# Performance work log

Measured on AMD Instinct MI355X. Metric: run time of the kernel, lower is better.

## Reference

```python
import jax, jax.numpy as jnp
import numpy as np

# loss weights (match init_kwargs)
L_M, L_U, L_B, L_D = 1.0, 7.0, 2.0, 1.0
NV, NP, NI, NB = 500_000, 64, 48, 2  # voxels, predictions, instances, batches


def setup_inputs() -> dict:
    key = jax.random.key(0)
    k1, k2 = jax.random.split(key)
    logits = jax.random.normal(k1, (NV, NP), dtype=jnp.float32)
    # sorted batch ids per voxel (first half batch 0, second half batch 1)
    voxel_batch = (jnp.arange(NV) * NB // NV).astype(jnp.int32)
    per_b = NI // NB
    # instance ids consistent with voxel batch (module assumes one batch per instance)
    gt_ids = (voxel_batch * per_b + jax.random.randint(k2, (NV,), 0, per_b)).astype(jnp.int32)
    centroid_batches = (jnp.arange(NP) * NB // NP).astype(jnp.int32)
    return {"logits": logits, "voxel_batch": voxel_batch, "gt_ids": gt_ids,
            "centroid_batches": centroid_batches}


def linear_sum_assignment(cost):
    """Hungarian algorithm (e-maxx JV variant) on a small numpy cost matrix."""
    cost = np.asarray(cost, dtype=np.float64)
    transposed = cost.shape[0] > cost.shape[1]
    C = cost.T if transposed else cost
    n, m = C.shape
    u = np.zeros(n + 1); v = np.zeros(m + 1)
    p = np.zeros(m + 1, dtype=np.int64); way = np.zeros(m + 1, dtype=np.int64)
    for i in range(1, n + 1):
        p[0] = i; j0 = 0
        minv = np.full(m + 1, np.inf); used = np.zeros(m + 1, dtype=bool)
        while True:
            used[j0] = True
            i0 = p[j0]; j1 = 0; delta = np.inf
            for j in range(1, m + 1):
                if not used[j]:
                    cur = C[i0 - 1, j - 1] - u[i0] - v[j]
                    if cur < minv[j]:
                        minv[j] = cur; way[j] = j0
                    if minv[j] < delta:
                        delta = minv[j]; j1 = j
            for j in range(m + 1):
                if used[j]:
                    u[p[j]] += delta; v[j] -= delta
                else:
                    minv[j] -= delta
            j0 = j1
            if p[j0] == 0:
                break
        while j0:
            j1 = way[j0]; p[j0] = p[j1]; j0 = j1
    ans = np.zeros(n, dtype=np.int64)
    for j in range(1, m + 1):
        if p[j] > 0:
            ans[p[j] - 1] = j - 1
    rows, cols = np.arange(n), ans
    if transposed:
        rows, cols = cols, rows
    order = np.argsort(rows)
    return rows[order], cols[order]


def reference(logits, voxel_batch, gt_ids, centroid_batches):
    vb = np.asarray(voxel_batch); gi = np.asarray(gt_ids); cb = np.asarray(centroid_batches)
    batches = np.unique(vb)
    uniq, inv = np.unique(gi, return_inverse=True)
    uniq_batches = np.zeros(uniq.size, dtype=np.int64)
    uniq_batches[inv] = vb  # batch id per unique GT instance
    losses = jnp.zeros(5, dtype=logits.dtype)
    for b in batches:
        vox = np.nonzero(vb == b)[0]
        pidx = np.nonzero(cb == b)[0]
        gidx = np.nonzero(uniq_batches == b)[0]
        if pidx.size == 0:
            continue
        x = logits[jnp.asarray(vox)][:, jnp.asarray(pidx)].T          # [P, Nv_b]
        g = (jnp.asarray(gi[vox])[None, :] == jnp.asarray(uniq[gidx])[:, None]).astype(logits.dtype)  # [G, Nv_b]
        # matcher pairwise costs (mean BCE + dice)
        pos = jnp.logaddexp(0.0, -x)  # BCE(x, 1) per element
        neg = jnp.logaddexp(0.0, x)   # BCE(x, 0) per element
        nvb = x.shape[1]
        cost_bce = (pos @ g.T + neg @ (1.0 - g).T) / nvb              # [P, G]
        p = jax.nn.sigmoid(x)
        cost_dice = 1.0 - (2.0 * (p @ g.T) + 1.0) / (p.sum(1)[:, None] + g.sum(1)[None, :] + 1.0)
        cost = L_B * cost_bce + L_D * cost_dice
        pr, gr = linear_sum_assignment(np.asarray(cost))
        G = g.shape[0]
        xm = x[jnp.asarray(pr)]; gm = g[jnp.asarray(gr)]              # matched pairs
        bce = L_B * (jnp.logaddexp(0.0, xm) - xm * gm).mean(1).sum() / G
        pm = jax.nn.sigmoid(xm)
        dice = L_D * (1.0 - (2.0 * (pm * gm).sum(1) + 1.0) / (pm.sum(1) + gm.sum(1) + 1.0)).sum() / G
        matched = L_M * (bce + dice)
        um = np.setdiff1d(np.arange(x.shape[0]), pr)
        if um.size:
            xu = x[jnp.asarray(um)]
            pu = jax.nn.sigmoid(xu)
            # sigmoid focal loss vs zeros: alpha_t=0.75, (1-p_t)^2 = p^2, ce = softplus(x)
            unmatched = L_U * (0.75 * jnp.logaddexp(0.0, xu) * pu * pu).mean()
        else:
            unmatched = jnp.zeros((), logits.dtype)
        total = matched + unmatched
        losses = losses + jnp.stack([total, matched, unmatched, bce, dice])
    return losses / batches.size  # [total, matched, unmatched, bce, dice]
```

## Files before the change

### kernel.cpp

```cpp
#include <hip/hip_runtime.h>
#include <math.h>

#define PB 32
#define GB 24
#define NBUK 48
#define NH 256
#define SL 16
#define PART 160

__global__ __launch_bounds__(256) void k_hist(const int* __restrict__ gi, int NV,
                                              int* __restrict__ counts)
{
    __shared__ int h[NBUK];
    int t = threadIdx.x;
    if (t < NBUK) h[t] = 0;
    __syncthreads();
    int CH = (NV + NH - 1) / NH;
    int lo = blockIdx.x * CH, hi = lo + CH; if (hi > NV) hi = NV;
    for (int i = lo + t; i < hi; i += 256) atomicAdd(&h[gi[i]], 1);
    __syncthreads();
    if (t < NBUK) counts[t * NH + blockIdx.x] = h[t];
}

__global__ __launch_bounds__(1024) void k_scan(const int* __restrict__ counts,
                                               int* __restrict__ offs, int* __restrict__ bs)
{
    __shared__ int tot[NBUK];
    __shared__ int bstart[NBUK + 1];
    int t = threadIdx.x, w = t >> 6, lane = t & 63;
    int c[3][4]; int excl[3];
    #pragma unroll
    for (int q = 0; q < 3; ++q) {
        int g = w * 3 + q;
        int base = g * NH + lane * 4;
        int s = 0;
        #pragma unroll
        for (int j = 0; j < 4; ++j) { c[q][j] = counts[base + j]; s += c[q][j]; }
        int inc = s;
        for (int off = 1; off < 64; off <<= 1) {
            int v = __shfl_up(inc, off);
            if (lane >= off) inc += v;
        }
        excl[q] = inc - s;
        int rt = __shfl(inc, 63);
        if (lane == 0) tot[g] = rt;
    }
    __syncthreads();
    if (t == 0) {
        int acc = 0;
        for (int g = 0; g < NBUK; ++g) { bstart[g] = acc; acc += tot[g]; }
        bstart[NBUK] = acc;
        for (int g = 0; g <= NBUK; ++g) bs[g] = bstart[g];
    }
    __syncthreads();
    #pragma unroll
    for (int q = 0; q < 3; ++q) {
        int g = w * 3 + q;
        int run = excl[q] + bstart[g];
        #pragma unroll
        for (int j = 0; j < 4; ++j) { offs[g * NH + lane * 4 + j] = run; run += c[q][j]; }
    }
}

__global__ __launch_bounds__(256) void k_scatter(const int* __restrict__ gi, int NV,
                                                 const int* __restrict__ offs,
                                                 int* __restrict__ sidx)
{
    __shared__ int cur[NBUK];
    __shared__ int wcnt[4][NBUK];
    int t = threadIdx.x, w = t >> 6, lane = t & 63;
    if (t < NBUK) cur[t] = offs[t * NH + blockIdx.x];
    int CH = (NV + NH - 1) / NH;
    int lo = blockIdx.x * CH, hi = lo + CH; if (hi > NV) hi = NV;
    unsigned long long below = (lane == 0) ? 0ull : ((~0ull) >> (64 - lane));

    for (int base = lo; base < hi; base += 256) {
        int v = base + t;
        bool act = (v < hi);
        int g = act ? gi[v] : -1;
        for (int j = t; j < 4 * NBUK; j += 256) (&wcnt[0][0])[j] = 0;
        __syncthreads();
        int rank_in_wave = 0;
        for (int q = 0; q < NBUK; ++q) {
            unsigned long long m = __ballot(g == q);
            if (m) {
                if (g == q) rank_in_wave = __popcll(m & below);
                if (lane == __ffsll((unsigned long long)m) - 1) wcnt[w][q] = __popcll(m);
            }
        }
        __syncthreads();
        if (act) {
            int pre = 0;
            for (int ww = 0; ww < w; ++ww) pre += wcnt[ww][g];
            sidx[cur[g] + pre + rank_in_wave] = v;
        }
        __syncthreads();
        if (t < NBUK) {
            int s = 0;
            for (int ww = 0; ww < 4; ++ww) s += wcnt[ww][t];
            cur[t] += s;
        }
        __syncthreads();
    }
}

__global__ __launch_bounds__(256) void k_accum2(
    const float* __restrict__ logits, const int* __restrict__ sidx,
    const int* __restrict__ bs, float* __restrict__ partials)
{
    int g = blockIdx.x >> 4, s = blockIdx.x & 15;
    int b = (g >= GB) ? 1 : 0;
    int lo = bs[g], hi = bs[g + 1];
    int sz = hi - lo;
    int sl = (sz + SL - 1) / SL;
    int p0 = lo + s * sl, p1 = p0 + sl; if (p1 > hi) p1 = hi;

    int t = threadIdx.x, w = t >> 6, lane = t & 63;
    int vi = lane >> 3, c0 = (lane & 7) * 4;
    int wn = p1 - p0;
    int wl = (wn + 3) / 4;
    int q0 = p0 + w * wl, q1 = q0 + wl; if (q1 > p1) q1 = p1;

    const float* xb = logits + 32 * b + c0;
    float sx[4] = {0,0,0,0}, sg[4] = {0,0,0,0};
    float tn[4] = {0,0,0,0}, ts[4] = {0,0,0,0}, tf[4] = {0,0,0,0};

    #pragma unroll 2
    for (int pos = q0; pos < q1; pos += 8) {
        int pv = pos + vi;
        if (pv < q1) {
            int idx = sidx[pv];
            float4 xq = *(const float4*)(xb + (size_t)idx * 64);
            float xs[4] = {xq.x, xq.y, xq.z, xq.w};
            #pragma unroll
            for (int e = 0; e < 4; ++e) {
                float x  = xs[e];
                float ax = fabsf(x);
                float ex = __expf(-ax);
                float neg = fmaxf(x, 0.f) + __logf(1.f + ex);
                float r  = __builtin_amdgcn_rcpf(1.f + ex);
                float sig = (x >= 0.f) ? r : ex * r;
                sx[e] += x;
                sg[e] += sig;
                tn[e] += neg;
                ts[e] += sig;
                tf[e] += neg * sig * sig;
            }
        }
    }

    #pragma unroll
    for (int off = 8; off <= 32; off <<= 1) {
        #pragma unroll
        for (int e = 0; e < 4; ++e) {
            sx[e] += __shfl_xor(sx[e], off);
            sg[e] += __shfl_xor(sg[e], off);
            tn[e] += __shfl_xor(tn[e], off);
            ts[e] += __shfl_xor(ts[e], off);
            tf[e] += __shfl_xor(tf[e], off);
        }
    }

    __shared__ float red[4][5][PB];
    if (lane < 8) {
        #pragma unroll
        for (int e = 0; e < 4; ++e) {
            red[w][0][c0 + e] = sx[e];
            red[w][1][c0 + e] = sg[e];
            red[w][2][c0 + e] = tn[e];
            red[w][3][c0 + e] = ts[e];
            red[w][4][c0 + e] = tf[e];
        }
    }
    __syncthreads();
    float* op = partials + (size_t)blockIdx.x * PART;
    for (int j = t; j < PART; j += 256)
        op[j] = (&red[0][0][0])[j] + (&red[1][0][0])[j] + (&red[2][0][0])[j] + (&red[3][0][0])[j];
}

#define DPPMIN(ctrl) { int tdp = __builtin_amdgcn_update_dpp(vbits, vbits, ctrl, 0xf, 0xf, false); \
    vbits = __float_as_int(fminf(__int_as_float(vbits), __int_as_float(tdp))); }
__device__ __forceinline__ float wave_min64(float x) {
    int vbits = __float_as_int(x);
    DPPMIN(0x111); DPPMIN(0x112); DPPMIN(0x114); DPPMIN(0x118);
    float a = __int_as_float(__builtin_amdgcn_readlane(vbits, 15));
    float b = __int_as_float(__builtin_amdgcn_readlane(vbits, 31));
    float c = __int_as_float(__builtin_amdgcn_readlane(vbits, 47));
    float d = __int_as_float(__builtin_amdgcn_readlane(vbits, 63));
    return fminf(fminf(a, b), fminf(c, d));
}

__global__ __launch_bounds__(1024) void k_final(
    const float* __restrict__ partials, const int* __restrict__ bs, float* __restrict__ outp)
{
    __shared__ float fs2[NBUK][5][PB];
    __shared__ float tneg[2][PB], tsig[2][PB], tfoc[2][PB];
    __shared__ float cntf[NBUK];
    __shared__ float nvbs[2];
    __shared__ float Ct[2][GB][PB];
    __shared__ float uincr[2][GB];
    __shared__ double bres[2][3];

    int tid = threadIdx.x;
    for (int j = tid; j < NBUK * PART; j += 1024) {
        int g = j / PART, r = j % PART;
        const float* base = partials + (size_t)g * SL * PART + r;
        float s = 0.f;
        #pragma unroll
        for (int k = 0; k < SL; ++k) s += base[(size_t)k * PART];
        (&fs2[0][0][0])[j] = s;
    }
    if (tid < NBUK) cntf[tid] = (float)(bs[tid + 1] - bs[tid]);
    __syncthreads();

    if (tid < 64) {
        int b = tid >> 5, p = tid & 31;
        float a = 0.f, c = 0.f, d = 0.f;
        for (int i = 0; i < GB; ++i) {
            a += fs2[b*GB + i][2][p];
            c += fs2[b*GB + i][3][p];
            d += fs2[b*GB + i][4][p];
        }
        tneg[b][p] = a; tsig[b][p] = c; tfoc[b][p] = d;
    }
    if (tid >= 64 && tid < 66) {
        int b = tid - 64; float s = 0.f;
        for (int i = 0; i < GB; ++i) s += cntf[b*GB + i];
        nvbs[b] = s;
    }
    __syncthreads();

    for (int idx = tid; idx < 2*GB*PB; idx += 1024) {
        int b = idx / (GB*PB), r = idx % (GB*PB), i = r / PB, j = r % PB;
        float nv = nvbs[b];
        float sx   = fs2[b*GB + i][0][j];
        float ssig = fs2[b*GB + i][1][j];
        float bceC  = 2.0f * (tneg[b][j] - sx) / nv;
        float diceC = 1.0f - (2.f*ssig + 1.f) / (tsig[b][j] + cntf[b*GB + i] + 1.f);
        Ct[b][i][j] = bceC + diceC;
    }
    __syncthreads();

    int p_final = 0;
    int wave = tid >> 6;
    int lane = tid & 63;
    if (tid < 128) {
        int b = wave;
        int j = lane;
        bool valid = (j >= 1 && j <= PB);
        float u_reg = 0.f;
        float v_reg = 0.f;
        int   p_reg = 0;

        for (int i = 1; i <= GB; ++i) {
            float Mv = 3e38f;
            int   way_reg = 0;
            bool  used = (lane == 0);
            float Duse = 0.f;
            if (lane == 0) p_reg = i;
            if (lane < GB) uincr[b][lane] = 0.f;
            int j0 = 0;
            float D = 0.f;
            for (int it = 0; it < 2*PB + 4; ++it) {
                int i0 = __builtin_amdgcn_readlane(p_reg, j0);
                float u0 = __int_as_float(__builtin_amdgcn_readlane(__float_as_int(u_reg), i0 - 1));
                float Crow = valid ? Ct[b][i0-1][j-1] : 0.f;
                float cur = Crow - u0 - v_reg + D;
                if (valid && !used && cur < Mv) { Mv = cur; way_reg = j0; }
                float cand = (valid && !used) ? Mv : 3e38f;
                float dm = wave_min64(cand);
                unsigned long long msk = __ballot(cand == dm);
                int j1 = (int)__ffsll(msk) - 1;
                D = dm;
                if (lane == j1) { used = true; Duse = dm; }
                j0 = j1;
                int pj0 = __builtin_amdgcn_readlane(p_reg, j0);
                if (pj0 == 0) break;
            }
            if (used) {
                v_reg -= (D - Duse);
                uincr[b][p_reg - 1] = D - Duse;
            }
            int jj = j0;
            for (int g2 = 0; g2 < PB + 2 && jj; ++g2) {
                int j1 = __builtin_amdgcn_readlane(way_reg, jj);
                int pj1 = __builtin_amdgcn_readlane(p_reg, j1);
                if (lane == jj) p_reg = pj1;
                jj = j1;
            }
            if (lane < GB) u_reg += uincr[b][lane];
        }
        p_final = p_reg;

        double nvbd = (double)nvbs[b];
        double myb = 0.0, myd = 0.0, myf = 0.0, myu = 0.0;
        if (valid) {
            int pj = p_final;
            int p = j - 1;
            if (pj > 0) {
                int ii = pj - 1;
                myb = ((double)tneg[b][p] - (double)fs2[b*GB + ii][0][p]) / nvbd;
                myd = 1.0 - (2.0*(double)fs2[b*GB + ii][1][p] + 1.0) /
                            ((double)tsig[b][p] + (double)cntf[b*GB + ii] + 1.0);
            } else {
                myf = (double)tfoc[b][p];
                myu = 1.0;
            }
        }
        #pragma unroll
        for (int off = 32; off >= 1; off >>= 1) {
            myb += __shfl_xor(myb, off);
            myd += __shfl_xor(myd, off);
            myf += __shfl_xor(myf, off);
            myu += __shfl_xor(myu, off);
        }
        if (lane == 0) {
            double G = (double)GB;
            double bce  = 2.0 * myb / G;
            double dice = 1.0 * myd / G;
            double unm  = (myu > 0.0) ? 7.0 * 0.75 * myf / (myu * nvbd)
                                      : 0.0;
            bres[b][0] = bce; bres[b][1] = dice; bres[b][2] = unm;
        }
    }
    __syncthreads();

    if (tid == 0) {
        double L[5] = {0,0,0,0,0};
        for (int b = 0; b < 2; ++b) {
            double bce = bres[b][0], dice = bres[b][1], unm = bres[b][2];
            double matched = bce + dice;
            double total = matched + unm;
            L[0] += total; L[1] += matched; L[2] += unm; L[3] += bce; L[4] += dice;
        }
        for (int k2 = 0; k2 < 5; ++k2) outp[k2] = (float)(L[k2] / 2.0);
    }
}

extern "C" void kernel_launch(void* const* d_in, const int* in_sizes, int n_in,
                              void* d_out, int out_size, void* d_ws, size_t ws_size,
                              hipStream_t stream)
{
    const float* logits = (const float*)d_in[0];
    const int* gi = (const int*)d_in[2];
    int NV = in_sizes[1];

    int* wsi = (int*)d_ws;
    int* counts = wsi;
    int* offs   = counts + NBUK * NH;
    int* bs     = offs + NBUK * NH;
    int* sidx   = bs + 64;
    float* partials = (float*)(sidx + NV);

    hipLaunchKernelGGL(k_hist,    dim3(NH), dim3(256), 0, stream, gi, NV, counts);
    hipLaunchKernelGGL(k_scan,    dim3(1), dim3(1024), 0, stream, counts, offs, bs);
    hipLaunchKernelGGL(k_scatter, dim3(NH), dim3(256), 0, stream, gi, NV, offs, sidx);
    hipLaunchKernelGGL(k_accum2,  dim3(NBUK * SL), dim3(256), 0, stream, logits, sidx, bs, partials);
    hipLaunchKernelGGL(k_final,   dim3(1), dim3(1024), 0, stream, partials, bs, (float*)d_out);
}
```

Before: 100.6 us.

## Add Hungarian dual init with greedy zero matching, register-cached costs, batch-bounded scatter ballots

The scatter kernel now limits its per-wave ballot loop to the instance buckets of the block's batch, using the sorted batch layout, which roughly halves the ballot iterations. In the final kernel, each lane keeps its cost column in registers and selects a row through a branchless tree instead of reading shared memory. Before the augmenting loop, the row and column duals are initialised from minima and zero-reduced-cost pairs are greedily matched, so those rows skip the serial Hungarian search. The assignment could differ when ties occur, and the extra register pressure could spill.

Measured after the change: 113.9 us. +13.3%, slower.

```diff
diff --git a/kernel.cpp b/kernel.cpp
--- a/kernel.cpp
+++ b/kernel.cpp
@@ -72,6 +72,8 @@
     if (t < NBUK) cur[t] = offs[t * NH + blockIdx.x];
     int CH = (NV + NH - 1) / NH;
     int lo = blockIdx.x * CH, hi = lo + CH; if (hi > NV) hi = NV;
+    int qlo = (gi[lo] >= GB) ? GB : 0;
+    int qhi = (gi[hi - 1] >= GB) ? NBUK : GB;
     unsigned long long below = (lane == 0) ? 0ull : ((~0ull) >> (64 - lane));
 
     for (int base = lo; base < hi; base += 256) {
@@ -81,7 +83,7 @@
         for (int j = t; j < 4 * NBUK; j += 256) (&wcnt[0][0])[j] = 0;
         __syncthreads();
         int rank_in_wave = 0;
-        for (int q = 0; q < NBUK; ++q) {
+        for (int q = qlo; q < qhi; ++q) {
             unsigned long long m = __ballot(g == q);
             if (m) {
                 if (g == q) rank_in_wave = __popcll(m & below);
@@ -95,7 +97,7 @@
             sidx[cur[g] + pre + rank_in_wave] = v;
         }
         __syncthreads();
-        if (t < NBUK) {
+        if (t >= qlo && t < qhi) {
             int s = 0;
             for (int ww = 0; ww < 4; ++ww) s += wcnt[ww][t];
             cur[t] += s;
@@ -190,6 +192,20 @@
     return fminf(fminf(a, b), fminf(c, d));
 }
 
+__device__ __forceinline__ float sel24(const float (&c)[GB], int k) {
+    float a[12];
+    #pragma unroll
+    for (int i = 0; i < 12; ++i) a[i] = (k & 1) ? c[2*i+1] : c[2*i];
+    float b2[6];
+    #pragma unroll
+    for (int i = 0; i < 6; ++i) b2[i] = (k & 2) ? a[2*i+1] : a[2*i];
+    float d[3];
+    #pragma unroll
+    for (int i = 0; i < 3; ++i) d[i] = (k & 4) ? b2[2*i+1] : b2[2*i];
+    float e0 = (k & 8) ? d[1] : d[0];
+    return (k & 16) ? d[2] : e0;
+}
+
 __global__ __launch_bounds__(1024) void k_final(
     const float* __restrict__ partials, const int* __restrict__ bs, float* __restrict__ outp)
 {
@@ -241,18 +257,45 @@
     }
     __syncthreads();
 
-    int p_final = 0;
     int wave = tid >> 6;
     int lane = tid & 63;
     if (tid < 128) {
         int b = wave;
         int j = lane;
         bool valid = (j >= 1 && j <= PB);
+
+        float creg[GB];
+        #pragma unroll
+        for (int i = 0; i < GB; ++i) creg[i] = valid ? Ct[b][i][j-1] : 3e38f;
+
         float u_reg = 0.f;
-        float v_reg = 0.f;
+        float us[GB];
+        #pragma unroll
+        for (int i = 0; i < GB; ++i) {
+            float rm = wave_min64(creg[i]);
+            us[i] = rm;
+            if (lane == i) u_reg = rm;
+        }
+        float vv = 3e38f;
+        #pragma unroll
+        for (int i = 0; i < GB; ++i) vv = fminf(vv, creg[i] - us[i]);
+        float v_reg = valid ? vv : 0.f;
         int   p_reg = 0;
 
+        unsigned rowdone = 0;
+        #pragma unroll
+        for (int i = 0; i < GB; ++i) {
+            bool z = valid && (p_reg == 0) && ((creg[i] - us[i] - v_reg) == 0.f);
+            unsigned long long m = __ballot(z);
+            if (m != 0ull) {
+                int js = (int)__ffsll(m) - 1;
+                if (lane == js) p_reg = i + 1;
+                rowdone |= (1u << i);
+            }
+        }
+
         for (int i = 1; i <= GB; ++i) {
+            if (rowdone & (1u << (i - 1))) continue;
             float Mv = 3e38f;
             int   way_reg = 0;
             bool  used = (lane == 0);
@@ -264,7 +307,7 @@
             for (int it = 0; it < 2*PB + 4; ++it) {
                 int i0 = __builtin_amdgcn_readlane(p_reg, j0);
                 float u0 = __int_as_float(__builtin_amdgcn_readlane(__float_as_int(u_reg), i0 - 1));
-                float Crow = valid ? Ct[b][i0-1][j-1] : 0.f;
+                float Crow = valid ? sel24(creg, i0 - 1) : 0.f;
                 float cur = Crow - u0 - v_reg + D;
                 if (valid && !used && cur < Mv) { Mv = cur; way_reg = j0; }
                 float cand = (valid && !used) ? Mv : 3e38f;
@@ -279,7 +322,7 @@
             }
             if (used) {
                 v_reg -= (D - Duse);
-                uincr[b][p_reg - 1] = D - Duse;
+                if (p_reg > 0) uincr[b][p_reg - 1] = D - Duse;
             }
             int jj = j0;
             for (int g2 = 0; g2 < PB + 2 && jj; ++g2) {
@@ -290,12 +333,11 @@
             }
             if (lane < GB) u_reg += uincr[b][lane];
         }
-        p_final = p_reg;
 
         double nvbd = (double)nvbs[b];
         double myb = 0.0, myd = 0.0, myf = 0.0, myu = 0.0;
         if (valid) {
-            int pj = p_final;
+            int pj = p_reg;
             int p = j - 1;
             if (pj > 0) {
                 int ii = pj - 1;
```
